# Kernel tuning notes

Hardware: AMD Instinct MI355X
Metric: run time of the kernel (lower is better)

## Reference

```python
import jax, jax.numpy as jnp
import numpy as np

C = 512      # channels
COND = 256   # cond_dim
H = 8        # n_heads
D = C // H   # head_dim
EPS = 1e-5


def setup_inputs() -> dict:
    key = jax.random.key(0)
    ks = jax.random.split(key, 16)
    s = 0.02
    inp = {
        "x": jax.random.normal(ks[0], (8, C, 1024), jnp.float32),
        "cond": jax.random.normal(ks[1], (8, COND), jnp.float32),
        "ln_g": jnp.ones((C,), jnp.float32),
        "ln_b": jnp.zeros((C,), jnp.float32),
        "Wq": jax.random.normal(ks[2], (C, C), jnp.float32) * s,
        "bq": jnp.zeros((C,), jnp.float32),
        "Wk": jax.random.normal(ks[3], (C, COND), jnp.float32) * s,
        "bk": jnp.zeros((C,), jnp.float32),
        "Wv": jax.random.normal(ks[4], (C, COND), jnp.float32) * s,
        "bv": jnp.zeros((C,), jnp.float32),
        "in_proj_w": jax.random.normal(ks[5], (3 * C, C), jnp.float32) * s,
        "in_proj_b": jnp.zeros((3 * C,), jnp.float32),
        "out_w": jax.random.normal(ks[6], (C, C), jnp.float32) * s,
        "out_b": jnp.zeros((C,), jnp.float32),
        "proj_w": jax.random.normal(ks[7], (C, C), jnp.float32) * s,
        "proj_b": jnp.zeros((C,), jnp.float32),
    }
    return inp


def _forward(x, cond, ln_g, ln_b, Wq, bq, Wk, bk, Wv, bv,
             in_proj_w, in_proj_b, out_w, out_b, proj_w, proj_b):
    B, _, T = x.shape
    x_seq = jnp.transpose(x, (0, 2, 1))                      # [B,T,C]
    mu = jnp.mean(x_seq, axis=-1, keepdims=True)
    var = jnp.mean((x_seq - mu) ** 2, axis=-1, keepdims=True)
    x_norm = (x_seq - mu) / jnp.sqrt(var + EPS) * ln_g + ln_b

    q = x_norm @ Wq.T + bq                                   # [B,T,C]
    k = cond @ Wk.T + bk                                     # [B,C]
    v = cond @ Wv.T + bv                                     # [B,C]

    # nn.MultiheadAttention internal input projections
    wq2, wk2, wv2 = in_proj_w[:C], in_proj_w[C:2 * C], in_proj_w[2 * C:]
    bq2, bk2, bv2 = in_proj_b[:C], in_proj_b[C:2 * C], in_proj_b[2 * C:]
    q2 = q @ wq2.T + bq2                                     # [B,T,C]
    k2 = k @ wk2.T + bk2                                     # [B,C]
    v2 = v @ wv2.T + bv2                                     # [B,C]

    qh = q2.reshape(B, T, H, D)                              # [B,T,H,D]
    kh = k2.reshape(B, H, D)
    vh = v2.reshape(B, H, D)

    # k/v are expanded to length T in the original module -> [B,T,C]
    k_exp = jnp.broadcast_to(kh[:, None, :, :], (B, T, H, D))
    v_exp = jnp.broadcast_to(vh[:, None, :, :], (B, T, H, D))

    scale = 1.0 / jnp.sqrt(jnp.float32(D))
    scores = jnp.einsum('bthd,bshd->bhts', qh * scale, k_exp)  # [B,H,T,T]
    attn = jax.nn.softmax(scores, axis=-1)
    outh = jnp.einsum('bhts,bshd->bthd', attn, v_exp)          # [B,T,H,D]
    out = outh.reshape(B, T, C) @ out_w.T + out_b              # MHA out_proj

    out = out @ proj_w.T + proj_b                              # self.proj
    out = jnp.transpose(out, (0, 2, 1))                        # [B,C,T]
    return x + out


def reference(x, cond, ln_g, ln_b, Wq, bq, Wk, bk, Wv, bv,
              in_proj_w, in_proj_b, out_w, out_b, proj_w, proj_b):
    return _forward(x, cond, ln_g, ln_b, Wq, bq, Wk, bk, Wv, bv,
                    in_proj_w, in_proj_b, out_w, out_b, proj_w, proj_b)
```

## Files before the change

kernel.cpp:

```cpp
#include <hip/hip_runtime.h>

#define CC 512
#define CK 256
#define BB 8
#define TT 1024
#define POSTRIDE (CC * CC)

__device__ __forceinline__ float wave_allreduce(float v) {
#pragma unroll
    for (int m = 1; m < 64; m <<= 1) v += __shfl_xor(v, m, 64);
    return v;
}
__device__ __forceinline__ float dot4(float4 a, float4 b) {
    return a.x * b.x + a.y * b.y + a.z * b.z + a.w * b.w;
}

__global__ void __launch_bounds__(256)
d1_kernel(const float* __restrict__ P, const float* __restrict__ O,
          const float* __restrict__ Wv, const float* __restrict__ bv,
          const float* __restrict__ ob, const float* __restrict__ pb,
          const float* __restrict__ cond,
          float* __restrict__ POpart, float* __restrict__ v1,
          float* __restrict__ t2)
{
    const int blk = blockIdx.x, tid = threadIdx.x;
    const int lane = tid & 63, wvid = tid >> 6;

    if (blk < 256) {
        __shared__ float As[64][36];
        __shared__ float Bs[32][68];
        const int kc = blk >> 6, t = blk & 63;
        const int ti = t >> 3, tj = t & 7;
        const int ty = tid >> 4, tx = tid & 15;
        const int ar = tid >> 3, ac4 = (tid & 7) * 4;
        const int br = tid >> 4, bc4 = (tid & 15) * 4;
        float acc[4][4] = {};

        int kb = kc * 128;
        float4 a0 = *(const float4*)&P[(size_t)(ti * 64 + ar) * CC + kb + ac4];
        float4 a1 = *(const float4*)&P[(size_t)(ti * 64 + 32 + ar) * CC + kb + ac4];
        float4 b0 = *(const float4*)&O[(size_t)(kb + br) * CC + tj * 64 + bc4];
        float4 b1 = *(const float4*)&O[(size_t)(kb + 16 + br) * CC + tj * 64 + bc4];

        for (int ch = 0; ch < 4; ++ch) {
            __syncthreads();
            *(float4*)&As[ar][ac4] = a0;
            *(float4*)&As[32 + ar][ac4] = a1;
            *(float4*)&Bs[br][bc4] = b0;
            *(float4*)&Bs[16 + br][bc4] = b1;
            __syncthreads();
            if (ch < 3) {
                kb = kc * 128 + (ch + 1) * 32;
                a0 = *(const float4*)&P[(size_t)(ti * 64 + ar) * CC + kb + ac4];
                a1 = *(const float4*)&P[(size_t)(ti * 64 + 32 + ar) * CC + kb + ac4];
                b0 = *(const float4*)&O[(size_t)(kb + br) * CC + tj * 64 + bc4];
                b1 = *(const float4*)&O[(size_t)(kb + 16 + br) * CC + tj * 64 + bc4];
            }
#pragma unroll
            for (int kk = 0; kk < 32; ++kk) {
                const float a_0 = As[4 * ty + 0][kk];
                const float a_1 = As[4 * ty + 1][kk];
                const float a_2 = As[4 * ty + 2][kk];
                const float a_3 = As[4 * ty + 3][kk];
                const float4 bq = *(const float4*)&Bs[kk][4 * tx];
                acc[0][0] += a_0 * bq.x; acc[0][1] += a_0 * bq.y;
                acc[0][2] += a_0 * bq.z; acc[0][3] += a_0 * bq.w;
                acc[1][0] += a_1 * bq.x; acc[1][1] += a_1 * bq.y;
                acc[1][2] += a_1 * bq.z; acc[1][3] += a_1 * bq.w;
                acc[2][0] += a_2 * bq.x; acc[2][1] += a_2 * bq.y;
                acc[2][2] += a_2 * bq.z; acc[2][3] += a_2 * bq.w;
                acc[3][0] += a_3 * bq.x; acc[3][1] += a_3 * bq.y;
                acc[3][2] += a_3 * bq.z; acc[3][3] += a_3 * bq.w;
            }
        }
        float* dst = POpart + (size_t)kc * POSTRIDE +
                     (size_t)(ti * 64 + 4 * ty) * CC + tj * 64 + 4 * tx;
#pragma unroll
        for (int i = 0; i < 4; ++i) {
            float4 v = { acc[i][0], acc[i][1], acc[i][2], acc[i][3] };
            *(float4*)&dst[(size_t)i * CC] = v;
        }
    } else if (blk < 1280) {
        const int row = (blk - 256) * 4 + wvid;
        const int b = row >> 9, c = row & 511;
        const float4 wv = *(const float4*)&Wv[(size_t)c * CK + lane * 4];
        const float4 cd = *(const float4*)&cond[b * CK + lane * 4];
        const float s = wave_allreduce(dot4(wv, cd));
        if (lane == 0) v1[row] = s + bv[c];
    } else {
        const int c = (blk - 1280) * 4 + wvid;
        const float4 pa = *(const float4*)&P[(size_t)c * CC + lane * 4];
        const float4 pc = *(const float4*)&P[(size_t)c * CC + CK + lane * 4];
        const float4 oa = *(const float4*)&ob[lane * 4];
        const float4 oc = *(const float4*)&ob[CK + lane * 4];
        const float s = wave_allreduce(dot4(pa, oa) + dot4(pc, oc));
        if (lane == 0) t2[c] = s + pb[c];
    }
}

__global__ void __launch_bounds__(256)
d2_kernel(const float* __restrict__ W2, const float* __restrict__ b2,
          const float* __restrict__ v1, float* __restrict__ v2)
{
    const int tid = threadIdx.x, lane = tid & 63;
    const int row = blockIdx.x * 4 + (tid >> 6);
    const int b = row >> 9, c = row & 511;
    const float4 wa = *(const float4*)&W2[(size_t)c * CC + lane * 4];
    const float4 wb = *(const float4*)&W2[(size_t)c * CC + CK + lane * 4];
    const float4 va = *(const float4*)&v1[b * CC + lane * 4];
    const float4 vb = *(const float4*)&v1[b * CC + CK + lane * 4];
    const float s = wave_allreduce(dot4(wa, va) + dot4(wb, vb));
    if (lane == 0) v2[row] = s + b2[c];
}

__global__ void __launch_bounds__(256)
stream_kernel(const float* __restrict__ x, const float* __restrict__ POpart,
              const float* __restrict__ t2, const float* __restrict__ v2,
              float* __restrict__ out)
{
    const int tid = threadIdx.x, lane = tid & 63;
    const int row = blockIdx.x * 4 + (tid >> 6);
    const int b = row >> 9, c = row & 511;

    const float4* x4 = (const float4*)x + (size_t)row * (TT / 4);
    float4 xr[4];
#pragma unroll
    for (int i = 0; i < 4; ++i) xr[i] = x4[i * 64 + lane];

    const float4 ua = *(const float4*)&v2[b * CC + lane * 4];
    const float4 ub = *(const float4*)&v2[b * CC + CK + lane * 4];
    float acc = 0.f;
#pragma unroll
    for (int p = 0; p < 4; ++p) {
        const float* prow = POpart + (size_t)p * POSTRIDE + (size_t)c * CC;
        const float4 pa = *(const float4*)&prow[lane * 4];
        const float4 pc = *(const float4*)&prow[CK + lane * 4];
        acc += dot4(pa, ua) + dot4(pc, ub);
    }
    const float w = wave_allreduce(acc) + t2[c];

    float4* o4 = (float4*)out + (size_t)row * (TT / 4);
#pragma unroll
    for (int i = 0; i < 4; ++i) {
        float4 v = xr[i];
        v.x += w; v.y += w; v.z += w; v.w += w;
        o4[i * 64 + lane] = v;
    }
}

extern "C" void kernel_launch(void* const* d_in, const int* in_sizes, int n_in,
                              void* d_out, int out_size, void* d_ws, size_t ws_size,
                              hipStream_t stream) {
    const float* x    = (const float*)d_in[0];
    const float* cond = (const float*)d_in[1];
    const float* Wv   = (const float*)d_in[8];
    const float* bv   = (const float*)d_in[9];
    const float* W2   = (const float*)d_in[10] + 2 * CC * CC;
    const float* b2   = (const float*)d_in[11] + 2 * CC;
    const float* O    = (const float*)d_in[12];
    const float* ob   = (const float*)d_in[13];
    const float* P    = (const float*)d_in[14];
    const float* pb   = (const float*)d_in[15];
    float* out = (float*)d_out;

    float* POpart = (float*)d_ws;
    float* v1 = POpart + 4 * POSTRIDE;
    float* v2 = v1 + BB * CC;
    float* t2 = v2 + BB * CC;

    d1_kernel<<<1408, 256, 0, stream>>>(P, O, Wv, bv, ob, pb, cond, POpart, v1, t2);
    d2_kernel<<<1024, 256, 0, stream>>>(W2, b2, v1, v2);
    stream_kernel<<<1024, 256, 0, stream>>>(x, POpart, t2, v2, out);
}
```

Measured before the change: 22.95 us.

## Fuse value-projection chain into first kernel, dropping separate d2 launch

The v1 = Wv·cond and v2 = W2·v1 matvecs move into 64 dedicated blocks of d1_kernel. Each block recomputes the full 512-entry v1 vector for its batch in shared memory, then produces a 64-row slice of v2. This removes one kernel launch and the global round trip of v1. In exchange, each block redundantly reads all of Wv (eight blocks per batch), and these 64 blocks run a longer serial loop that may become the critical path of d1.

Result: slower. 39.53 us (+72.2%).

```diff
diff --git a/kernel.cpp b/kernel.cpp
--- a/kernel.cpp
+++ b/kernel.cpp
@@ -18,18 +18,58 @@
 __global__ void __launch_bounds__(256)
 d1_kernel(const float* __restrict__ P, const float* __restrict__ O,
           const float* __restrict__ Wv, const float* __restrict__ bv,
+          const float* __restrict__ W2, const float* __restrict__ b2,
           const float* __restrict__ ob, const float* __restrict__ pb,
           const float* __restrict__ cond,
-          float* __restrict__ POpart, float* __restrict__ v1,
+          float* __restrict__ POpart, float* __restrict__ v2g,
           float* __restrict__ t2)
 {
     const int blk = blockIdx.x, tid = threadIdx.x;
     const int lane = tid & 63, wvid = tid >> 6;
 
-    if (blk < 256) {
+    if (blk < 64) {
+        __shared__ float v1s[CC];
+        const int b = blk >> 3, c0 = (blk & 7) * 64;
+        const float4 cd = *(const float4*)&cond[b * CK + lane * 4];
+        for (int r = 0; r < 128; r += 4) {
+            const int row = wvid * 128 + r;
+            float s0 = dot4(*(const float4*)&Wv[(size_t)(row + 0) * CK + lane * 4], cd);
+            float s1 = dot4(*(const float4*)&Wv[(size_t)(row + 1) * CK + lane * 4], cd);
+            float s2 = dot4(*(const float4*)&Wv[(size_t)(row + 2) * CK + lane * 4], cd);
+            float s3 = dot4(*(const float4*)&Wv[(size_t)(row + 3) * CK + lane * 4], cd);
+            s0 = wave_allreduce(s0); s1 = wave_allreduce(s1);
+            s2 = wave_allreduce(s2); s3 = wave_allreduce(s3);
+            if (lane == 0) {
+                v1s[row + 0] = s0 + bv[row + 0];
+                v1s[row + 1] = s1 + bv[row + 1];
+                v1s[row + 2] = s2 + bv[row + 2];
+                v1s[row + 3] = s3 + bv[row + 3];
+            }
+        }
+        __syncthreads();
+        const float4 va = *(const float4*)&v1s[lane * 4];
+        const float4 vb = *(const float4*)&v1s[CK + lane * 4];
+        for (int r = 0; r < 16; r += 4) {
+            const int c = c0 + wvid * 16 + r;
+            float s[4];
+#pragma unroll
+            for (int i = 0; i < 4; ++i) {
+                const float4 wa = *(const float4*)&W2[(size_t)(c + i) * CC + lane * 4];
+                const float4 wb = *(const float4*)&W2[(size_t)(c + i) * CC + CK + lane * 4];
+                s[i] = dot4(wa, va) + dot4(wb, vb);
+            }
+#pragma unroll
+            for (int i = 0; i < 4; ++i) s[i] = wave_allreduce(s[i]);
+            if (lane == 0) {
+#pragma unroll
+                for (int i = 0; i < 4; ++i) v2g[b * CC + c + i] = s[i] + b2[c + i];
+            }
+        }
+    } else if (blk < 320) {
         __shared__ float As[64][36];
         __shared__ float Bs[32][68];
-        const int kc = blk >> 6, t = blk & 63;
+        const int g = blk - 64;
+        const int kc = g >> 6, t = g & 63;
         const int ti = t >> 3, tj = t & 7;
         const int ty = tid >> 4, tx = tid & 15;
         const int ar = tid >> 3, ac4 = (tid & 7) * 4;
@@ -80,15 +120,8 @@
             float4 v = { acc[i][0], acc[i][1], acc[i][2], acc[i][3] };
             *(float4*)&dst[(size_t)i * CC] = v;
         }
-    } else if (blk < 1280) {
-        const int row = (blk - 256) * 4 + wvid;
-        const int b = row >> 9, c = row & 511;
-        const float4 wv = *(const float4*)&Wv[(size_t)c * CK + lane * 4];
-        const float4 cd = *(const float4*)&cond[b * CK + lane * 4];
-        const float s = wave_allreduce(dot4(wv, cd));
-        if (lane == 0) v1[row] = s + bv[c];
     } else {
-        const int c = (blk - 1280) * 4 + wvid;
+        const int c = (blk - 320) * 4 + wvid;
         const float4 pa = *(const float4*)&P[(size_t)c * CC + lane * 4];
         const float4 pc = *(const float4*)&P[(size_t)c * CC + CK + lane * 4];
         const float4 oa = *(const float4*)&ob[lane * 4];
@@ -96,21 +129,6 @@
         const float s = wave_allreduce(dot4(pa, oa) + dot4(pc, oc));
         if (lane == 0) t2[c] = s + pb[c];
     }
-}
-
-__global__ void __launch_bounds__(256)
-d2_kernel(const float* __restrict__ W2, const float* __restrict__ b2,
-          const float* __restrict__ v1, float* __restrict__ v2)
-{
-    const int tid = threadIdx.x, lane = tid & 63;
-    const int row = blockIdx.x * 4 + (tid >> 6);
-    const int b = row >> 9, c = row & 511;
-    const float4 wa = *(const float4*)&W2[(size_t)c * CC + lane * 4];
-    const float4 wb = *(const float4*)&W2[(size_t)c * CC + CK + lane * 4];
-    const float4 va = *(const float4*)&v1[b * CC + lane * 4];
-    const float4 vb = *(const float4*)&v1[b * CC + CK + lane * 4];
-    const float s = wave_allreduce(dot4(wa, va) + dot4(wb, vb));
-    if (lane == 0) v2[row] = s + b2[c];
 }
 
 __global__ void __launch_bounds__(256)
@@ -164,11 +182,10 @@
     float* out = (float*)d_out;
 
     float* POpart = (float*)d_ws;
-    float* v1 = POpart + 4 * POSTRIDE;
-    float* v2 = v1 + BB * CC;
+    float* v2 = POpart + 4 * POSTRIDE;
     float* t2 = v2 + BB * CC;
 
-    d1_kernel<<<1408, 256, 0, stream>>>(P, O, Wv, bv, ob, pb, cond, POpart, v1, t2);
-    d2_kernel<<<1024, 256, 0, stream>>>(W2, b2, v1, v2);
+    d1_kernel<<<448, 256, 0, stream>>>(P, O, Wv, bv, W2, b2, ob, pb, cond,
+                                       POpart, v2, t2);
     stream_kernel<<<1024, 256, 0, stream>>>(x, POpart, t2, v2, out);
 }
```
